# Performance work log

Measured on AMD Instinct MI355X. Metric: run time of the kernel, lower is better.

## Reference

```python
import math
import jax, jax.numpy as jnp
import numpy as np

HEADS = 8


def setup_inputs() -> dict:
    key = jax.random.key(0)
    ks = jax.random.split(key, 8)
    B, L, S, C = 2, 1024, 2048, 1280
    CORR = 256  # native seg_corr resolution; nearest-upsampled x4 to (1024, 1024)
    sc = 0.02
    return {
        "hidden_states": jax.random.normal(ks[0], (B, L, C), jnp.float32),
        "encoder_hidden_states": jax.random.normal(ks[1], (B, S, C), jnp.float32),
        "seg_corr": jax.random.randint(ks[2], (B, CORR, CORR), 0, 2, jnp.int32),
        "Wq": jax.random.normal(ks[3], (C, C), jnp.float32) * sc,
        "Wk": jax.random.normal(ks[4], (C, C), jnp.float32) * sc,
        "Wv": jax.random.normal(ks[5], (C, C), jnp.float32) * sc,
        "Wo": jax.random.normal(ks[6], (C, C), jnp.float32) * sc,
        "bo": jnp.zeros((C,), jnp.float32),
    }


def reference(hidden_states, encoder_hidden_states, seg_corr, Wq, Wk, Wv, Wo, bo):
    B, L, C = hidden_states.shape
    S = encoder_hidden_states.shape[1]
    H = HEADS
    d = C // H

    # projections -> [B, H, L, d] / [B, H, S, d]
    q = (hidden_states @ Wq).reshape(B, L, H, d).transpose(0, 2, 1, 3)
    k = (encoder_hidden_states @ Wk).reshape(B, S, H, d).transpose(0, 2, 1, 3)
    v = (encoder_hidden_states @ Wv).reshape(B, S, H, d).transpose(0, 2, 1, 3)

    scale = 1.0 / math.sqrt(d)
    scores = jnp.einsum("bhld,bhsd->bhls", q, k) * scale  # [B, H, L, S]

    half = S // 2  # S == 2L in the match-attention branch
    # nearest-neighbor upsample of seg_corr to (L, half) == integer repeat
    rL = L // seg_corr.shape[1]
    rS = half // seg_corr.shape[2]
    corr = jnp.repeat(jnp.repeat(seg_corr, rL, axis=1), rS, axis=2)[:, None]  # [B,1,L,half]

    # hard correlation mask on the second half of keys (reference-image tokens)
    masked = jnp.where(corr == 1, scores[..., half:], jnp.float32(-jnp.inf))
    scores = jnp.concatenate([scores[..., :half], masked], axis=-1)

    attn_weight = jax.nn.softmax(scores, axis=-1)  # dropout_p = 0.0
    out = jnp.einsum("bhls,bhsd->bhld", attn_weight, v)
    out = out.transpose(0, 2, 1, 3).reshape(B, L, C)

    out = out @ Wo + bo            # to_out[0]; to_out[1] dropout is identity at p=0
    out = out + hidden_states      # residual connection; rescale_output_factor = 1
    return out
```

## Files before the change

kernel.cpp:

```cpp
#include <hip/hip_runtime.h>

typedef unsigned short u16;
typedef unsigned int   u32;
typedef unsigned char  u8;

using bf16x8 = __attribute__((ext_vector_type(8))) __bf16;
using f32x4  = __attribute__((ext_vector_type(4))) float;
using s16x4  = __attribute__((ext_vector_type(4))) short;

__device__ __forceinline__ u16 f2bf(float f) {
    u32 u = __float_as_uint(f);
    return (u16)((u + 0x7FFFu + ((u >> 16) & 1u)) >> 16);
}

#define MFMA(a, b, c) __builtin_amdgcn_mfma_f32_16x16x32_bf16((a), (b), (c), 0, 0, 0)
#define MFMA16(a, b, c) __builtin_amdgcn_mfma_f32_16x16x16bf16_1k((a), (b), (c), 0, 0, 0)

__device__ __forceinline__ void gll16(const u16* g, u16* l) {
    __builtin_amdgcn_global_load_lds(
        (const __attribute__((address_space(1))) void*)g,
        (__attribute__((address_space(3))) void*)l, 16, 0, 0);
}

__global__ __launch_bounds__(256) void wtrans_kernel(
    const float* __restrict__ W0, const float* __restrict__ W1,
    const float* __restrict__ W2, const float* __restrict__ W3,
    u16* __restrict__ T0, u16* __restrict__ T1,
    u16* __restrict__ T2, u16* __restrict__ T3) {
    const int N = 1280;
    const int z = blockIdx.z;
    const float* W = (z == 0) ? W0 : (z == 1) ? W1 : (z == 2) ? W2 : W3;
    u16* T = (z == 0) ? T0 : (z == 1) ? T1 : (z == 2) ? T2 : T3;
    __shared__ float t[32][33];
    const int bx = blockIdx.x * 32, by = blockIdx.y * 32;
    const int x = threadIdx.x, ty = threadIdx.y;
#pragma unroll
    for (int j = 0; j < 4; j++) {
        const int y = ty + j * 8;
        t[y][x] = W[(size_t)(by + y) * N + (bx + x)];
    }
    __syncthreads();
#pragma unroll
    for (int j = 0; j < 4; j++) {
        const int y = ty + j * 8;
        T[(size_t)(bx + y) * N + (by + x)] = f2bf(t[x][y]);
    }
}

__global__ __launch_bounds__(256) void conv_kernel(const float* __restrict__ in,
                                                   u16* __restrict__ out, int n8) {
    const int i = blockIdx.x * 256 + threadIdx.x;
    if (i >= n8) return;
    const float4 a = ((const float4*)in)[i * 2];
    const float4 b = ((const float4*)in)[i * 2 + 1];
    union { uint4 u; u16 s[8]; } cv;
    cv.s[0] = f2bf(a.x); cv.s[1] = f2bf(a.y); cv.s[2] = f2bf(a.z); cv.s[3] = f2bf(a.w);
    cv.s[4] = f2bf(b.x); cv.s[5] = f2bf(b.y); cv.s[6] = f2bf(b.z); cv.s[7] = f2bf(b.w);
    ((uint4*)out)[i] = cv.u;
}

template <int MI, bool TRANSC, bool EPI>
__global__ __launch_bounds__(256) void gemm2_kernel(
    const u16* __restrict__ A, const u16* __restrict__ Bt, void* __restrict__ Cp,
    const float* __restrict__ bias, const float* __restrict__ resid,
    const int M, const int N, const int K) {
    __shared__ __align__(16) u16 Al[2][MI * 32 * 64];
    __shared__ __align__(16) u16 Bl[2][128 * 64];
    const int tid = threadIdx.x;
    const int lane = tid & 63, w = tid >> 6;
    const int wr = w >> 1, wc = w & 1;
    const int lr = lane & 15, lq = lane >> 4;
    const int m0 = blockIdx.y * (MI * 32), n0 = blockIdx.x * 128;

    const int f_r = tid >> 3;
    const int srcch = (tid & 7) ^ ((tid >> 3) & 7);
    const int ldst = (tid & 192) * 8;

    const f32x4 fzero = {0.f, 0.f, 0.f, 0.f};
    f32x4 acc[MI][4];
#pragma unroll
    for (int i = 0; i < MI; i++)
#pragma unroll
        for (int j = 0; j < 4; j++) acc[i][j] = fzero;

    const int nkt = K >> 6;

#define STAGE(buf, kt)                                                          \
    {                                                                           \
        const int k0s = (kt) << 6;                                              \
        _Pragma("unroll")                                                       \
        for (int i = 0; i < MI; i++) {                                          \
            const int r = i * 32 + f_r;                                         \
            gll16(&A[(size_t)(m0 + r) * K + k0s + srcch * 8],                   \
                  &Al[buf][i * 2048 + ldst]);                                   \
        }                                                                       \
        _Pragma("unroll")                                                       \
        for (int i = 0; i < 4; i++) {                                           \
            const int r = i * 32 + f_r;                                         \
            gll16(&Bt[(size_t)(n0 + r) * K + k0s + srcch * 8],                  \
                  &Bl[buf][i * 2048 + ldst]);                                   \
        }                                                                       \
    }

    STAGE(0, 0);
    asm volatile("s_waitcnt vmcnt(0)" ::: "memory");
    __syncthreads();
    int cur = 0;
    for (int kt = 0; kt < nkt; kt++) {
        if (kt + 1 < nkt) STAGE(cur ^ 1, kt + 1);
#pragma unroll
        for (int ks = 0; ks < 2; ks++) {
            bf16x8 af[MI], bfv[4];
#pragma unroll
            for (int mi = 0; mi < MI; mi++) {
                const int rowA = wr * (MI * 16) + mi * 16 + lr;
                af[mi] = *(const bf16x8*)&Al[cur][rowA * 64 +
                                                  (((ks * 4 + lq) ^ (rowA & 7)) << 3)];
            }
#pragma unroll
            for (int ni = 0; ni < 4; ni++) {
                const int rowB = wc * 64 + ni * 16 + lr;
                bfv[ni] = *(const bf16x8*)&Bl[cur][rowB * 64 +
                                                   (((ks * 4 + lq) ^ (rowB & 7)) << 3)];
            }
#pragma unroll
            for (int mi = 0; mi < MI; mi++)
#pragma unroll
                for (int ni = 0; ni < 4; ni++)
                    acc[mi][ni] = MFMA(af[mi], bfv[ni], acc[mi][ni]);
        }
        asm volatile("s_waitcnt vmcnt(0)" ::: "memory");
        __syncthreads();
        cur ^= 1;
    }
#undef STAGE

#pragma unroll
    for (int mi = 0; mi < MI; mi++)
#pragma unroll
        for (int ni = 0; ni < 4; ni++)
#pragma unroll
            for (int j = 0; j < 4; j++) {
                const int row = m0 + wr * (MI * 16) + mi * 16 + lq * 4 + j;
                const int col = n0 + wc * 64 + ni * 16 + lr;
                const float v = acc[mi][ni][j];
                if (EPI) {
                    ((float*)Cp)[(size_t)row * N + col] =
                        v + bias[col] + resid[(size_t)row * N + col];
                } else if (TRANSC) {
                    ((u16*)Cp)[((size_t)(col >> 11) * 1280 + row) * 2048 +
                               (col & 2047)] = f2bf(v);
                } else {
                    ((u16*)Cp)[(size_t)row * N + col] = f2bf(v);
                }
            }
}

__global__ __launch_bounds__(256) void attn_kernel(
    const u16* __restrict__ qb, const u16* __restrict__ kb,
    const u16* __restrict__ vtb, const int* __restrict__ seg,
    u16* __restrict__ ao) {
    __shared__ __align__(16) u16 arena[20224];
    const int KL = 0;
    const int VT = 10752;
    const int PT = 17152;
    const int SG = 18944;
    const int ML = 19968;
    u8* segl8 = (u8*)&arena[SG];
    float* Mlf = (float*)&arena[ML];
    float* Osum = (float*)&arena[KL];

    const int tid = threadIdx.x;
    const int lane = tid & 63, w = tid >> 6;
    const int qg = w >> 1, kc = w & 1;
    const int lr = lane & 15, lq = lane >> 4;
    const int id = blockIdx.x;
    const int h = id & 7, bz = (id >> 3) & 1, qt = id >> 4;

#pragma unroll
    for (int i = 0; i < 2; i++) {
        const int4 v =
            *(const int4*)&seg[(size_t)(bz * 256 + qt * 8) * 256 + tid * 8 + i * 4];
        segl8[tid * 8 + i * 4 + 0] = (u8)v.x;
        segl8[tid * 8 + i * 4 + 1] = (u8)v.y;
        segl8[tid * 8 + i * 4 + 2] = (u8)v.z;
        segl8[tid * 8 + i * 4 + 3] = (u8)v.w;
    }

    bf16x8 qf[5];
    {
        const size_t qrow =
            (size_t)(bz * 1024 + qt * 32 + qg * 16 + lr) * 1280 + h * 160;
#pragma unroll
        for (int ks = 0; ks < 5; ks++)
            qf[ks] = *(const bf16x8*)&qb[qrow + ks * 32 + lq * 8];
    }

    const int nk0 = tid, nk1 = tid + 256;
    const int nv0 = tid, nv1 = tid + 256;
    const bool exK = (tid < 128);
    const int ne = exK ? (512 + tid) : (512 + tid - 128);
    const int gok0 = (nk0 / 20) * 1280 + (nk0 % 20) * 8;
    const int lok0 = (nk0 / 20) * 168 + (nk0 % 20) * 8;
    const int gok1 = (nk1 / 20) * 1280 + (nk1 % 20) * 8;
    const int lok1 = (nk1 / 20) * 168 + (nk1 % 20) * 8;
    const int gov0 = (nv0 >> 2) * 2048 + (nv0 & 3) * 8;
    const int lov0 = (nv0 >> 2) * 40 + (nv0 & 3) * 8;
    const int gov1 = (nv1 >> 2) * 2048 + (nv1 & 3) * 8;
    const int lov1 = (nv1 >> 2) * 40 + (nv1 & 3) * 8;
    const int goe = exK ? ((ne / 20) * 1280 + (ne % 20) * 8)
                        : ((ne >> 2) * 2048 + (ne & 3) * 8);
    const int loe = exK ? ((ne / 20) * 168 + (ne % 20) * 8)
                        : ((ne >> 2) * 40 + (ne & 3) * 8);

    const u16* kT = kb + (size_t)(bz * 2048) * 1280 + h * 160;
    const u16* vT = vtb + (size_t)(bz * 1280 + h * 160) * 2048;

    const f32x4 fzero = {0.f, 0.f, 0.f, 0.f};
    f32x4 oacc[10];
#pragma unroll
    for (int d = 0; d < 10; d++) oacc[d] = fzero;
    f32x4 oaccL = fzero;
    float m_i[4] = {0.f, 0.f, 0.f, 0.f};
    const float sc = 0.07905694150420949f;
    const s16x4 ones = {(short)0x3F80, (short)0x3F80, (short)0x3F80, (short)0x3F80};
    u16* ptw = &arena[PT + w * 448];

    uint4 rk0 = *(const uint4*)&kT[gok0];
    uint4 rk1 = *(const uint4*)&kT[gok1];
    uint4 rv0 = *(const uint4*)&vT[gov0];
    uint4 rv1 = *(const uint4*)&vT[gov1];
    uint4 re  = exK ? *(const uint4*)&kT[goe] : *(const uint4*)&vT[goe];

    for (int kt = 0; kt < 64; kt++) {
        __syncthreads();
        *(uint4*)&arena[KL + lok0] = rk0;
        *(uint4*)&arena[KL + lok1] = rk1;
        *(uint4*)&arena[VT + lov0] = rv0;
        *(uint4*)&arena[VT + lov1] = rv1;
        if (exK) *(uint4*)&arena[KL + loe] = re;
        else     *(uint4*)&arena[VT + loe] = re;
        if (kt + 1 < 64) {
            const u16* kTn = kT + (size_t)(kt + 1) * 40960;
            const u16* vTn = vT + (kt + 1) * 32;
            rk0 = *(const uint4*)&kTn[gok0];
            rk1 = *(const uint4*)&kTn[gok1];
            rv0 = *(const uint4*)&vTn[gov0];
            rv1 = *(const uint4*)&vTn[gov1];
            re  = exK ? *(const uint4*)&kTn[goe] : *(const uint4*)&vTn[goe];
        }
        __syncthreads();

        f32x4 s4 = fzero;
#pragma unroll
        for (int ks = 0; ks < 5; ks++) {
            const bf16x8 bk =
                *(const bf16x8*)&arena[KL + (kc * 16 + lr) * 168 + ks * 32 + lq * 8];
            s4 = MFMA(qf[ks], bk, s4);
        }
        float msk = 0.f;
        if (kt >= 32) {
            const int sg = (kt - 32) * 8 + kc * 4 + (lr >> 2);
            msk = segl8[(qg * 4 + lq) * 256 + sg] ? 0.f : -1e30f;
        }
#pragma unroll
        for (int j = 0; j < 4; j++) s4[j] = s4[j] * sc + msk;

        const bool ex = (s4[0] > m_i[0] + 8.f) || (s4[1] > m_i[1] + 8.f) ||
                        (s4[2] > m_i[2] + 8.f) || (s4[3] > m_i[3] + 8.f);
        if (__any(ex)) {
#pragma unroll
            for (int j = 0; j < 4; j++) {
                float rm = s4[j];
                rm = fmaxf(rm, __shfl_xor(rm, 1));
                rm = fmaxf(rm, __shfl_xor(rm, 2));
                rm = fmaxf(rm, __shfl_xor(rm, 4));
                rm = fmaxf(rm, __shfl_xor(rm, 8));
                const float mn = fmaxf(m_i[j], rm);
                const float al = __expf(m_i[j] - mn);
#pragma unroll
                for (int d = 0; d < 10; d++) oacc[d][j] *= al;
                oaccL[j] *= al;
                m_i[j] = mn;
            }
        }
#pragma unroll
        for (int j = 0; j < 4; j++) {
            const float e = __expf(s4[j] - m_i[j]);
            ptw[(lq * 4 + j) * 28 + lr] = f2bf(e);
        }
        const s16x4 pa = *(const s16x4*)&ptw[lr * 28 + lq * 4];
        oaccL = MFMA16(pa, ones, oaccL);
#pragma unroll
        for (int nt2 = 0; nt2 < 10; nt2++) {
            const s16x4 bv =
                *(const s16x4*)&arena[VT + (nt2 * 16 + lr) * 40 + kc * 16 + lq * 4];
            oacc[nt2] = MFMA16(pa, bv, oacc[nt2]);
        }
    }

    if (lr == 0) {
#pragma unroll
        for (int j = 0; j < 4; j++) {
            Mlf[(w * 16 + lq * 4 + j) * 2 + 0] = m_i[j];
            Mlf[(w * 16 + lq * 4 + j) * 2 + 1] = oaccL[j];
        }
    }
    __syncthreads();
    float aj[4], inv[4];
#pragma unroll
    for (int j = 0; j < 4; j++) {
        const int row = lq * 4 + j;
        const float m1 = Mlf[((w ^ 1) * 16 + row) * 2];
        const float l1 = Mlf[((w ^ 1) * 16 + row) * 2 + 1];
        const float M = fmaxf(m_i[j], m1);
        aj[j] = __expf(m_i[j] - M);
        inv[j] = 1.f / (oaccL[j] * aj[j] + l1 * __expf(m1 - M));
    }
    if (kc == 1) {
#pragma unroll
        for (int nt2 = 0; nt2 < 10; nt2++)
#pragma unroll
            for (int j = 0; j < 4; j++)
                Osum[(qg * 16 + lq * 4 + j) * 164 + nt2 * 16 + lr] =
                    oacc[nt2][j] * aj[j];
    }
    __syncthreads();
    if (kc == 0) {
#pragma unroll
        for (int nt2 = 0; nt2 < 10; nt2++)
#pragma unroll
            for (int j = 0; j < 4; j++) {
                const int row = lq * 4 + j;
                const float v = (oacc[nt2][j] * aj[j] +
                                 Osum[(qg * 16 + row) * 164 + nt2 * 16 + lr]) *
                                inv[j];
                ao[(size_t)(bz * 1024 + qt * 32 + qg * 16 + row) * 1280 + h * 160 +
                   nt2 * 16 + lr] = f2bf(v);
            }
    }
}

extern "C" void kernel_launch(void* const* d_in, const int* in_sizes, int n_in,
                              void* d_out, int out_size, void* d_ws, size_t ws_size,
                              hipStream_t stream) {
    const float* hs  = (const float*)d_in[0];
    const float* ehs = (const float*)d_in[1];
    const int*   seg = (const int*)d_in[2];
    const float* Wq  = (const float*)d_in[3];
    const float* Wk  = (const float*)d_in[4];
    const float* Wv  = (const float*)d_in[5];
    const float* Wo  = (const float*)d_in[6];
    const float* bo  = (const float*)d_in[7];
    float* out = (float*)d_out;

    u16* base  = (u16*)d_ws;
    u16* WoT   = base;
    u16* qbuf  = WoT + 1638400;
    u16* kbuf  = qbuf + 2621440;
    u16* vtbuf = kbuf + 5242880;
    u16* hbuf  = vtbuf + 5242880;
    u16* ebuf  = hbuf + 2621440;
    u16* WqT   = ebuf + 5242880;
    u16* WkT   = WqT + 1638400;
    u16* WvT   = WkT + 1638400;
    u16* aobuf = hbuf;

    dim3 tb(32, 8), tg(40, 40, 4);
    wtrans_kernel<<<tg, tb, 0, stream>>>(Wq, Wk, Wv, Wo, WqT, WkT, WvT, WoT);
    conv_kernel<<<1280, 256, 0, stream>>>(hs, hbuf, 327680);
    conv_kernel<<<2560, 256, 0, stream>>>(ehs, ebuf, 655360);

    gemm2_kernel<2, false, false><<<dim3(10, 32), 256, 0, stream>>>(
        hbuf, WqT, qbuf, nullptr, nullptr, 2048, 1280, 1280);
    gemm2_kernel<4, false, false><<<dim3(10, 32), 256, 0, stream>>>(
        ebuf, WkT, kbuf, nullptr, nullptr, 4096, 1280, 1280);
    gemm2_kernel<4, true, false><<<dim3(32, 10), 256, 0, stream>>>(
        WvT, ebuf, vtbuf, nullptr, nullptr, 1280, 4096, 1280);

    attn_kernel<<<512, 256, 0, stream>>>(qbuf, kbuf, vtbuf, seg, aobuf);

    gemm2_kernel<2, false, true><<<dim3(10, 32), 256, 0, stream>>>(
        aobuf, WoT, out, bo, hs, 2048, 1280, 1280);
}
```

Measured before the change: 190.8 us.

## Split attention over key halves with a merge kernel and fuse conversions

The attention kernel now splits the key sequence into two halves (split-K / flash-decoding style). This doubles the block count to 1024 and halves the loop length. Each half writes unnormalized bf16 partial outputs plus row max/sum, and a new merge kernel combines them with a rescale. The two input conversion launches are fused into one, and the QK MFMA chain is split into two accumulators to shorten the dependency chain. The change trades more parallelism and occupancy (less shared memory) for extra global traffic on the partials, another launch, and some bf16 rounding of unnormalized partials.

Result: slower. 199.8 us (+4.7%).

```diff
diff --git a/kernel.cpp b/kernel.cpp
--- a/kernel.cpp
+++ b/kernel.cpp
@@ -11,6 +11,9 @@
 __device__ __forceinline__ u16 f2bf(float f) {
     u32 u = __float_as_uint(f);
     return (u16)((u + 0x7FFFu + ((u >> 16) & 1u)) >> 16);
+}
+__device__ __forceinline__ float bf2f(u16 x) {
+    return __uint_as_float(((u32)x) << 16);
 }
 
 #define MFMA(a, b, c) __builtin_amdgcn_mfma_f32_16x16x32_bf16((a), (b), (c), 0, 0, 0)
@@ -47,10 +50,14 @@
     }
 }
 
-__global__ __launch_bounds__(256) void conv_kernel(const float* __restrict__ in,
-                                                   u16* __restrict__ out, int n8) {
-    const int i = blockIdx.x * 256 + threadIdx.x;
-    if (i >= n8) return;
+__global__ __launch_bounds__(256) void conv2_kernel(const float* __restrict__ in0,
+                                                    u16* __restrict__ out0,
+                                                    const float* __restrict__ in1,
+                                                    u16* __restrict__ out1) {
+    const int bid = blockIdx.x;
+    const float* in = (bid < 1280) ? in0 : in1;
+    u16* out = (bid < 1280) ? out0 : out1;
+    const int i = ((bid < 1280) ? bid : bid - 1280) * 256 + threadIdx.x;
     const float4 a = ((const float4*)in)[i * 2];
     const float4 b = ((const float4*)in)[i * 2 + 1];
     union { uint4 u; u16 s[8]; } cv;
@@ -159,13 +166,13 @@
 __global__ __launch_bounds__(256) void attn_kernel(
     const u16* __restrict__ qb, const u16* __restrict__ kb,
     const u16* __restrict__ vtb, const int* __restrict__ seg,
-    u16* __restrict__ ao) {
-    __shared__ __align__(16) u16 arena[20224];
+    u16* __restrict__ op, float* __restrict__ mlp) {
+    __shared__ __align__(16) u16 arena[14848];
     const int KL = 0;
-    const int VT = 10752;
-    const int PT = 17152;
-    const int SG = 18944;
-    const int ML = 19968;
+    const int VT = 5376;
+    const int PT = 11776;
+    const int SG = 13568;
+    const int ML = 14592;
     u8* segl8 = (u8*)&arena[SG];
     float* Mlf = (float*)&arena[ML];
     float* Osum = (float*)&arena[KL];
@@ -175,16 +182,18 @@
     const int qg = w >> 1, kc = w & 1;
     const int lr = lane & 15, lq = lane >> 4;
     const int id = blockIdx.x;
-    const int h = id & 7, bz = (id >> 3) & 1, qt = id >> 4;
-
-#pragma unroll
-    for (int i = 0; i < 2; i++) {
-        const int4 v =
-            *(const int4*)&seg[(size_t)(bz * 256 + qt * 8) * 256 + tid * 8 + i * 4];
-        segl8[tid * 8 + i * 4 + 0] = (u8)v.x;
-        segl8[tid * 8 + i * 4 + 1] = (u8)v.y;
-        segl8[tid * 8 + i * 4 + 2] = (u8)v.z;
-        segl8[tid * 8 + i * 4 + 3] = (u8)v.w;
+    const int h = id & 7, bz = (id >> 3) & 1, sp = (id >> 4) & 1, qt = id >> 5;
+
+    if (sp == 1) {
+#pragma unroll
+        for (int i = 0; i < 2; i++) {
+            const int4 v =
+                *(const int4*)&seg[(size_t)(bz * 256 + qt * 8) * 256 + tid * 8 + i * 4];
+            segl8[tid * 8 + i * 4 + 0] = (u8)v.x;
+            segl8[tid * 8 + i * 4 + 1] = (u8)v.y;
+            segl8[tid * 8 + i * 4 + 2] = (u8)v.z;
+            segl8[tid * 8 + i * 4 + 3] = (u8)v.w;
+        }
     }
 
     bf16x8 qf[5];
@@ -199,7 +208,7 @@
     const int nk0 = tid, nk1 = tid + 256;
     const int nv0 = tid, nv1 = tid + 256;
     const bool exK = (tid < 128);
-    const int ne = exK ? (512 + tid) : (512 + tid - 128);
+    const int ne = exK ? (512 + tid) : (384 + tid);
     const int gok0 = (nk0 / 20) * 1280 + (nk0 % 20) * 8;
     const int lok0 = (nk0 / 20) * 168 + (nk0 % 20) * 8;
     const int gok1 = (nk1 / 20) * 1280 + (nk1 % 20) * 8;
@@ -213,8 +222,8 @@
     const int loe = exK ? ((ne / 20) * 168 + (ne % 20) * 8)
                         : ((ne >> 2) * 40 + (ne & 3) * 8);
 
-    const u16* kT = kb + (size_t)(bz * 2048) * 1280 + h * 160;
-    const u16* vT = vtb + (size_t)(bz * 1280 + h * 160) * 2048;
+    const u16* kT = kb + (size_t)(bz * 2048 + sp * 1024) * 1280 + h * 160;
+    const u16* vT = vtb + (size_t)(bz * 1280 + h * 160) * 2048 + sp * 1024;
 
     const f32x4 fzero = {0.f, 0.f, 0.f, 0.f};
     f32x4 oacc[10];
@@ -232,7 +241,7 @@
     uint4 rv1 = *(const uint4*)&vT[gov1];
     uint4 re  = exK ? *(const uint4*)&kT[goe] : *(const uint4*)&vT[goe];
 
-    for (int kt = 0; kt < 64; kt++) {
+    for (int kt = 0; kt < 32; kt++) {
         __syncthreads();
         *(uint4*)&arena[KL + lok0] = rk0;
         *(uint4*)&arena[KL + lok1] = rk1;
@@ -240,7 +249,7 @@
         *(uint4*)&arena[VT + lov1] = rv1;
         if (exK) *(uint4*)&arena[KL + loe] = re;
         else     *(uint4*)&arena[VT + loe] = re;
-        if (kt + 1 < 64) {
+        if (kt + 1 < 32) {
             const u16* kTn = kT + (size_t)(kt + 1) * 40960;
             const u16* vTn = vT + (kt + 1) * 32;
             rk0 = *(const uint4*)&kTn[gok0];
@@ -251,20 +260,21 @@
         }
         __syncthreads();
 
-        f32x4 s4 = fzero;
-#pragma unroll
-        for (int ks = 0; ks < 5; ks++) {
-            const bf16x8 bk =
-                *(const bf16x8*)&arena[KL + (kc * 16 + lr) * 168 + ks * 32 + lq * 8];
-            s4 = MFMA(qf[ks], bk, s4);
-        }
         float msk = 0.f;
-        if (kt >= 32) {
-            const int sg = (kt - 32) * 8 + kc * 4 + (lr >> 2);
+        if (sp == 1) {
+            const int sg = kt * 8 + kc * 4 + (lr >> 2);
             msk = segl8[(qg * 4 + lq) * 256 + sg] ? 0.f : -1e30f;
         }
-#pragma unroll
-        for (int j = 0; j < 4; j++) s4[j] = s4[j] * sc + msk;
+
+        const u16* kbase = &arena[KL + (kc * 16 + lr) * 168 + lq * 8];
+        f32x4 s4 = fzero, s4b = fzero;
+        s4  = MFMA(qf[0], *(const bf16x8*)&kbase[0],   s4);
+        s4b = MFMA(qf[1], *(const bf16x8*)&kbase[32],  s4b);
+        s4  = MFMA(qf[2], *(const bf16x8*)&kbase[64],  s4);
+        s4b = MFMA(qf[3], *(const bf16x8*)&kbase[96],  s4b);
+        s4  = MFMA(qf[4], *(const bf16x8*)&kbase[128], s4);
+#pragma unroll
+        for (int j = 0; j < 4; j++) s4[j] = (s4[j] + s4b[j]) * sc + msk;
 
         const bool ex = (s4[0] > m_i[0] + 8.f) || (s4[1] > m_i[1] + 8.f) ||
                         (s4[2] > m_i[2] + 8.f) || (s4[3] > m_i[3] + 8.f);
@@ -307,7 +317,7 @@
         }
     }
     __syncthreads();
-    float aj[4], inv[4];
+    float aj[4], Lr[4], Mr[4];
 #pragma unroll
     for (int j = 0; j < 4; j++) {
         const int row = lq * 4 + j;
@@ -315,30 +325,57 @@
         const float l1 = Mlf[((w ^ 1) * 16 + row) * 2 + 1];
         const float M = fmaxf(m_i[j], m1);
         aj[j] = __expf(m_i[j] - M);
-        inv[j] = 1.f / (oaccL[j] * aj[j] + l1 * __expf(m1 - M));
+        Lr[j] = oaccL[j] * aj[j] + l1 * __expf(m1 - M);
+        Mr[j] = M;
     }
     if (kc == 1) {
 #pragma unroll
         for (int nt2 = 0; nt2 < 10; nt2++)
 #pragma unroll
             for (int j = 0; j < 4; j++)
-                Osum[(qg * 16 + lq * 4 + j) * 164 + nt2 * 16 + lr] =
+                Osum[(qg * 16 + lq * 4 + j) * 168 + nt2 * 16 + lr] =
                     oacc[nt2][j] * aj[j];
     }
     __syncthreads();
     if (kc == 0) {
 #pragma unroll
-        for (int nt2 = 0; nt2 < 10; nt2++)
-#pragma unroll
-            for (int j = 0; j < 4; j++) {
-                const int row = lq * 4 + j;
-                const float v = (oacc[nt2][j] * aj[j] +
-                                 Osum[(qg * 16 + row) * 164 + nt2 * 16 + lr]) *
-                                inv[j];
-                ao[(size_t)(bz * 1024 + qt * 32 + qg * 16 + row) * 1280 + h * 160 +
-                   nt2 * 16 + lr] = f2bf(v);
-            }
-    }
+        for (int j = 0; j < 4; j++) {
+            const int row = lq * 4 + j;
+            const size_t rg = (size_t)(bz * 1024 + qt * 32 + qg * 16 + row);
+            if (lr == 0) {
+                mlp[(((size_t)sp * 2048 + rg) * 8 + h) * 2 + 0] = Mr[j];
+                mlp[(((size_t)sp * 2048 + rg) * 8 + h) * 2 + 1] = Lr[j];
+            }
+#pragma unroll
+            for (int nt2 = 0; nt2 < 10; nt2++) {
+                const float v = oacc[nt2][j] * aj[j] +
+                                Osum[(qg * 16 + row) * 168 + nt2 * 16 + lr];
+                op[((size_t)sp * 2048 + rg) * 1280 + h * 160 + nt2 * 16 + lr] =
+                    f2bf(v);
+            }
+        }
+    }
+}
+
+__global__ __launch_bounds__(256) void merge2_kernel(const u16* __restrict__ op,
+                                                     const float* __restrict__ mlp,
+                                                     u16* __restrict__ ao) {
+    const int e = blockIdx.x * 256 + threadIdx.x;
+    const int r = e / 640, cp = e % 640;
+    const int h = cp / 80;
+    const float m0 = mlp[(((size_t)0 + r) * 8 + h) * 2 + 0];
+    const float l0 = mlp[(((size_t)0 + r) * 8 + h) * 2 + 1];
+    const float m1 = mlp[(((size_t)2048 + r) * 8 + h) * 2 + 0];
+    const float l1 = mlp[(((size_t)2048 + r) * 8 + h) * 2 + 1];
+    const float M = fmaxf(m0, m1);
+    const float a0 = __expf(m0 - M), a1 = __expf(m1 - M);
+    const float inv = 1.f / (l0 * a0 + l1 * a1);
+    const u32 p0 = *(const u32*)&op[((size_t)0 + r) * 1280 + cp * 2];
+    const u32 p1 = *(const u32*)&op[((size_t)2048 + r) * 1280 + cp * 2];
+    const float x0 = bf2f((u16)p0) * a0 + bf2f((u16)p1) * a1;
+    const float x1 = bf2f((u16)(p0 >> 16)) * a0 + bf2f((u16)(p1 >> 16)) * a1;
+    const u32 pk = (u32)f2bf(x0 * inv) | ((u32)f2bf(x1 * inv) << 16);
+    *(u32*)&ao[(size_t)r * 1280 + cp * 2] = pk;
 }
 
 extern "C" void kernel_launch(void* const* d_in, const int* in_sizes, int n_in,
@@ -364,12 +401,13 @@
     u16* WqT   = ebuf + 5242880;
     u16* WkT   = WqT + 1638400;
     u16* WvT   = WkT + 1638400;
-    u16* aobuf = hbuf;
+    u16* opart = hbuf;
+    float* mlpart = (float*)WqT;
+    u16* aobuf = qbuf;
 
     dim3 tb(32, 8), tg(40, 40, 4);
     wtrans_kernel<<<tg, tb, 0, stream>>>(Wq, Wk, Wv, Wo, WqT, WkT, WvT, WoT);
-    conv_kernel<<<1280, 256, 0, stream>>>(hs, hbuf, 327680);
-    conv_kernel<<<2560, 256, 0, stream>>>(ehs, ebuf, 655360);
+    conv2_kernel<<<3840, 256, 0, stream>>>(hs, hbuf, ehs, ebuf);
 
     gemm2_kernel<2, false, false><<<dim3(10, 32), 256, 0, stream>>>(
         hbuf, WqT, qbuf, nullptr, nullptr, 2048, 1280, 1280);
@@ -378,7 +416,8 @@
     gemm2_kernel<4, true, false><<<dim3(32, 10), 256, 0, stream>>>(
         WvT, ebuf, vtbuf, nullptr, nullptr, 1280, 4096, 1280);
 
-    attn_kernel<<<512, 256, 0, stream>>>(qbuf, kbuf, vtbuf, seg, aobuf);
+    attn_kernel<<<1024, 256, 0, stream>>>(qbuf, kbuf, vtbuf, seg, opart, mlpart);
+    merge2_kernel<<<5120, 256, 0, stream>>>(opart, mlpart, aobuf);
 
     gemm2_kernel<2, false, true><<<dim3(10, 32), 256, 0, stream>>>(
         aobuf, WoT, out, bo, hs, 2048, 1280, 1280);
```
